# Optimization experiments

Measured on AMD Instinct MI355X. Metric: run time of the kernel, lower is better.

Reference implementation:

```python
import jax, jax.numpy as jnp
import numpy as np

B, N, D, H = 4, 4096, 1024, 16
DK = D // H


def setup_inputs() -> dict:
    key = jax.random.key(0)
    ks = jax.random.split(key, 11)
    s = 0.02  # small init scale for weights
    return {
        "query": jax.random.normal(ks[0], (B, N, D), jnp.float32),
        "key": jax.random.normal(ks[1], (B, N, D), jnp.float32),
        "value": jax.random.normal(ks[2], (B, N, D), jnp.float32),
        "Wq": jax.random.normal(ks[3], (D, D), jnp.float32) * s,
        "bq": jax.random.normal(ks[4], (D,), jnp.float32) * s,
        "Wk": jax.random.normal(ks[5], (D, D), jnp.float32) * s,
        "bk": jax.random.normal(ks[6], (D,), jnp.float32) * s,
        "Wv": jax.random.normal(ks[7], (D, D), jnp.float32) * s,
        "bv": jax.random.normal(ks[8], (D,), jnp.float32) * s,
        "Wo": jax.random.normal(ks[9], (D, D), jnp.float32) * s,
        "bo": jax.random.normal(ks[10], (D,), jnp.float32) * s,
    }


def reference(query, key, value, Wq, bq, Wk, bk, Wv, bv, Wo, bo):
    b, n, d = query.shape
    h, dk = H, d // H

    def proj(x, W, bias):
        # torch Linear: y = x @ W.T + b ; then split heads -> [b,h,n,dk]
        y = x @ W.T + bias
        return y.reshape(b, n, h, dk).transpose(0, 2, 1, 3)

    q = proj(query, Wq, bq)
    k = proj(key, Wk, bk)
    v = proj(value, Wv, bv)

    # linear attention (Efficient Attention, arXiv:1812.01243)
    q = jax.nn.softmax(q, axis=-1) * (1.0 / np.sqrt(dk).astype(np.float32))
    k = jax.nn.softmax(k, axis=-2)  # softmax over sequence dim
    ctx = jnp.einsum('bhnd,bhne->bhde', k, v)   # [b,h,dk,dk]
    out = jnp.einsum('bhnd,bhde->bhne', q, ctx)  # [b,h,n,dk]

    out = out.transpose(0, 2, 1, 3).reshape(b, n, d)
    return out @ Wo.T + bo
```

## Files before the change

### kernel.cpp

```cpp
#include <hip/hip_runtime.h>
#include <hip/hip_bf16.h>

#define B_ 4
#define N_ 4096
#define D_ 1024
#define H_ 16

typedef __attribute__((ext_vector_type(4))) float f32x4;
typedef __attribute__((ext_vector_type(8))) short s16x8;

__device__ __forceinline__ ushort f2bf(float f) {
  union { float f; unsigned u; } v; v.f = f;
  unsigned u = v.u;
  return (ushort)((u + 0x7fffu + ((u >> 16) & 1u)) >> 16);
}
__device__ __forceinline__ float bf2f(ushort h) {
  union { unsigned u; float f; } v; v.u = ((unsigned)h) << 16;
  return v.f;
}

__device__ __forceinline__ void gld16(const ushort* g, ushort* lds_base) {
  __builtin_amdgcn_global_load_lds(
      (const __attribute__((address_space(1))) unsigned int*)g,
      (__attribute__((address_space(3))) unsigned int*)lds_base, 16, 0, 0);
}

__device__ __forceinline__ s16x8 cvt8(float4 a, float4 b) {
  s16x8 o;
  o[0] = (short)f2bf(a.x); o[1] = (short)f2bf(a.y); o[2] = (short)f2bf(a.z); o[3] = (short)f2bf(a.w);
  o[4] = (short)f2bf(b.x); o[5] = (short)f2bf(b.y); o[6] = (short)f2bf(b.z); o[7] = (short)f2bf(b.w);
  return o;
}

__global__ void conv_x_kernel(const float* __restrict__ x0, const float* __restrict__ x1,
                              const float* __restrict__ x2, ushort* __restrict__ dst) {
  const int z = blockIdx.z;
  const float* src = z == 0 ? x0 : (z == 1 ? x1 : x2);
  ushort* d = dst + (long)z * 16777216;
  const long i0 = ((long)blockIdx.x * 256 + threadIdx.x) * 8;
  const long STR = (long)1024 * 256 * 8;
  float4 va[8], vb[8];
#pragma unroll
  for (int u = 0; u < 8; ++u) {
    va[u] = *(const float4*)(src + i0 + u * STR);
    vb[u] = *(const float4*)(src + i0 + u * STR + 4);
  }
#pragma unroll
  for (int u = 0; u < 8; ++u) {
    *(s16x8*)(d + i0 + u * STR) = cvt8(va[u], vb[u]);
  }
}

__global__ void conv_w_kernel(const float* __restrict__ w0, const float* __restrict__ w1,
                              const float* __restrict__ w2, const float* __restrict__ w3,
                              ushort* __restrict__ dst) {
  const int z = blockIdx.z;
  const float* src = z == 0 ? w0 : z == 1 ? w1 : z == 2 ? w2 : w3;
  ushort* d = dst + (long)z * (D_ * D_);
  const long i0 = ((long)blockIdx.x * 256 + threadIdx.x) * 8;
  const long STR = (long)128 * 256 * 8;
  float4 va[4], vb[4];
#pragma unroll
  for (int u = 0; u < 4; ++u) {
    va[u] = *(const float4*)(src + i0 + u * STR);
    vb[u] = *(const float4*)(src + i0 + u * STR + 4);
  }
#pragma unroll
  for (int u = 0; u < 4; ++u) {
    *(s16x8*)(d + i0 + u * STR) = cvt8(va[u], vb[u]);
  }
}

template <int EPI>
__global__ __launch_bounds__(256, 2) void gemm_bt_kernel(
    const ushort* __restrict__ A, const ushort* __restrict__ Bm,
    void* __restrict__ Cv, const float* __restrict__ bias, float* __restrict__ kpart,
    int M, int N, int K, long sA, long sB, long sC) {
  __shared__ ushort As[128 * 32];
  __shared__ ushort Bs[128 * 32];
  const int z = blockIdx.z;
  A += (long)z * sA; Bm += (long)z * sB;
  const int m0 = blockIdx.x * 128, n0 = blockIdx.y * 128;
  const int tid = threadIdx.x;
  const int wave = tid >> 6, lane = tid & 63;
  const int fl = lane & 15, fh = lane >> 4;
  const int wm = wave >> 1, wn = wave & 1;
  f32x4 acc[4][4] = {};
  const int c0 = tid, c1 = tid + 256;
  const int r0 = c0 >> 2, k80 = (c0 & 3) * 8;
  const int r1 = c1 >> 2, k81 = (c1 & 3) * 8;
  ushort* ldsA0 = As + wave * 512;
  ushort* ldsA1 = As + 2048 + wave * 512;
  ushort* ldsB0 = Bs + wave * 512;
  ushort* ldsB1 = Bs + 2048 + wave * 512;
  for (int kk = 0; kk < K; kk += 32) {
    __syncthreads();
    gld16(A + (long)(m0 + r0) * K + kk + k80, ldsA0);
    gld16(A + (long)(m0 + r1) * K + kk + k81, ldsA1);
    gld16(Bm + (long)(n0 + r0) * K + kk + k80, ldsB0);
    gld16(Bm + (long)(n0 + r1) * K + kk + k81, ldsB1);
    __syncthreads();
    s16x8 fa[4], fb[4];
#pragma unroll
    for (int i = 0; i < 4; ++i)
      fa[i] = *(const s16x8*)(As + (wm * 64 + i * 16 + fl) * 32 + fh * 8);
#pragma unroll
    for (int j = 0; j < 4; ++j)
      fb[j] = *(const s16x8*)(Bs + (wn * 64 + j * 16 + fl) * 32 + fh * 8);
#pragma unroll
    for (int i = 0; i < 4; ++i)
#pragma unroll
      for (int j = 0; j < 4; ++j)
        acc[i][j] = __builtin_amdgcn_mfma_f32_16x16x32_bf16(fa[i], fb[j], acc[i][j], 0, 0, 0);
  }

  if constexpr (EPI == 0) {
    ushort* C = (ushort*)Cv;
#pragma unroll
    for (int j = 0; j < 4; ++j) {
      int col = n0 + wn * 64 + j * 16 + fl;
#pragma unroll
      for (int i = 0; i < 4; ++i)
#pragma unroll
        for (int r = 0; r < 4; ++r) {
          int row = m0 + wm * 64 + i * 16 + fh * 4 + r;
          C[(long)row * N + col] = f2bf(acc[i][j][r]);
        }
    }
  } else if constexpr (EPI == 1) {
    ushort* C = (ushort*)Cv;
    float bcol[4];
#pragma unroll
    for (int j = 0; j < 4; ++j) bcol[j] = bias[n0 + wn * 64 + j * 16 + fl];
#pragma unroll
    for (int i = 0; i < 4; ++i)
#pragma unroll
      for (int r = 0; r < 4; ++r) {
        float v[4];
#pragma unroll
        for (int j = 0; j < 4; ++j) v[j] = acc[i][j][r] + bcol[j];
        float m = fmaxf(fmaxf(v[0], v[1]), fmaxf(v[2], v[3]));
#pragma unroll
        for (int o = 1; o <= 8; o <<= 1) m = fmaxf(m, __shfl_xor(m, o));
        float e[4], s = 0.f;
#pragma unroll
        for (int j = 0; j < 4; ++j) { e[j] = __expf(v[j] - m); s += e[j]; }
#pragma unroll
        for (int o = 1; o <= 8; o <<= 1) s += __shfl_xor(s, o);
        float sc = 0.125f / s;
        int row = m0 + wm * 64 + i * 16 + fh * 4 + r;
#pragma unroll
        for (int j = 0; j < 4; ++j)
          C[(long)row * N + n0 + wn * 64 + j * 16 + fl] = f2bf(e[j] * sc);
      }
  } else if constexpr (EPI == 2) {
    ushort* C = (ushort*)Cv;
    float csum[4] = {};
#pragma unroll
    for (int j = 0; j < 4; ++j) {
      int col = n0 + wn * 64 + j * 16 + fl;
#pragma unroll
      for (int i = 0; i < 4; ++i)
#pragma unroll
        for (int r = 0; r < 4; ++r) {
          int row = m0 + wm * 64 + i * 16 + fh * 4 + r;
          float e = __expf(acc[i][j][r]);
          csum[j] += e;
          C[(long)row * N + col] = f2bf(e);
        }
    }
#pragma unroll
    for (int j = 0; j < 4; ++j) {
#pragma unroll
      for (int o = 16; o <= 32; o <<= 1) csum[j] += __shfl_xor(csum[j], o);
    }
    if (fh == 0) {
      int b = m0 >> 12;
      int chunk = ((m0 & 4095) >> 7) * 2 + wm;
#pragma unroll
      for (int j = 0; j < 4; ++j)
        kpart[(long)b * 65536 + (long)chunk * 1024 + n0 + wn * 64 + j * 16 + fl] = csum[j];
    }
  } else {
    float* C = (float*)Cv + (long)z * sC;
#pragma unroll
    for (int j = 0; j < 4; ++j) {
      int col = n0 + wn * 64 + j * 16 + fl;
      float bv = bias[col];
#pragma unroll
      for (int i = 0; i < 4; ++i)
#pragma unroll
        for (int r = 0; r < 4; ++r) {
          int row = m0 + wm * 64 + i * 16 + fh * 4 + r;
          C[(long)row * N + col] = acc[i][j][r] + bv;
        }
    }
  }
}

__global__ void ksm2_kernel(const float* __restrict__ kpart, float* __restrict__ colinv) {
  int idx = blockIdx.x * 256 + threadIdx.x;
  int b = idx >> 10, d = idx & 1023;
  float s = 0.f;
  for (int c = 0; c < 64; ++c) s += kpart[(long)b * 65536 + (long)c * 1024 + d];
  colinv[idx] = 1.0f / s;
}

__global__ __launch_bounds__(256, 2) void ctx_partial_kernel(
    const ushort* __restrict__ Ksm, const ushort* __restrict__ Vp, float* __restrict__ part) {
  __shared__ ushort Ks[128 * 64];
  __shared__ ushort Vs[128 * 64];
  const int chunk = blockIdx.x;
  const int bh = blockIdx.y;
  const int b = bh >> 4, h = bh & 15;
  const int tid = threadIdx.x, wave = tid >> 6, lane = tid & 63;
  const int fl = lane & 15, fh = lane >> 4;
  f32x4 acc[4] = {};
  for (int t = 0; t < 4; ++t) {
    const long base = ((long)(b * N_ + chunk * 512 + t * 128)) * D_ + h * 64;
    __syncthreads();
#pragma unroll
    for (int i = 0; i < 4; ++i) {
      int c = i * 256 + tid;
      int r = c >> 3, k8 = (c & 7) * 8;
      ushort* lk = Ks + (long)(i * 256 + wave * 64) * 8;
      ushort* lv = Vs + (long)(i * 256 + wave * 64) * 8;
      gld16(Ksm + base + (long)r * D_ + k8, lk);
      gld16(Vp + base + (long)r * D_ + k8, lv);
    }
    __syncthreads();
#pragma unroll
    for (int s = 0; s < 4; ++s) {
      s16x8 fa;
#pragma unroll
      for (int j = 0; j < 8; ++j)
        fa[j] = (short)Ks[(s * 32 + fh * 8 + j) * 64 + wave * 16 + fl];
#pragma unroll
      for (int jt = 0; jt < 4; ++jt) {
        s16x8 fb;
#pragma unroll
        for (int j = 0; j < 8; ++j)
          fb[j] = (short)Vs[(s * 32 + fh * 8 + j) * 64 + jt * 16 + fl];
        acc[jt] = __builtin_amdgcn_mfma_f32_16x16x32_bf16(fa, fb, acc[jt], 0, 0, 0);
      }
    }
  }
  float* dst = part + ((long)chunk * 64 + bh) * 4096;
#pragma unroll
  for (int jt = 0; jt < 4; ++jt)
#pragma unroll
    for (int r = 0; r < 4; ++r)
      dst[(wave * 16 + fh * 4 + r) * 64 + jt * 16 + fl] = acc[jt][r];
}

__global__ void ctx_reduce_kernel(const float* __restrict__ part, const float* __restrict__ bv,
                                  const float* __restrict__ colinv, ushort* __restrict__ ctxb) {
  int idx = blockIdx.x * 256 + threadIdx.x;
  int e = idx & 63;
  int dk = (idx >> 6) & 63;
  int h = (idx >> 12) & 15;
  int b = idx >> 16;
  float s = 0.f;
#pragma unroll
  for (int c = 0; c < 8; ++c) s += part[(long)c * 262144 + idx];
  ctxb[idx] = f2bf(s * colinv[b * 1024 + h * 64 + dk] + bv[h * 64 + e]);
}

__global__ __launch_bounds__(256, 2) void mb_kernel(
    const ushort* __restrict__ Wob, const ushort* __restrict__ ctxb, ushort* __restrict__ Mb) {
  const int o0 = blockIdx.x * 64, h = blockIdx.y, b = blockIdx.z;
  const int tid = threadIdx.x, wave = tid >> 6, lane = tid & 63;
  const int fl = lane & 15, fh = lane >> 4;
  const ushort* ctxh = ctxb + ((long)(b * 16 + h)) * 4096;
  f32x4 acc[4] = {};
#pragma unroll
  for (int s = 0; s < 2; ++s) {
    s16x8 fa = *(const s16x8*)(Wob + (long)(o0 + wave * 16 + fl) * D_ + h * 64 + s * 32 + fh * 8);
#pragma unroll
    for (int jt = 0; jt < 4; ++jt) {
      s16x8 fb = *(const s16x8*)(ctxh + (long)(jt * 16 + fl) * 64 + s * 32 + fh * 8);
      acc[jt] = __builtin_amdgcn_mfma_f32_16x16x32_bf16(fa, fb, acc[jt], 0, 0, 0);
    }
  }
  ushort* dst = Mb + (long)b * (D_ * D_);
#pragma unroll
  for (int jt = 0; jt < 4; ++jt)
#pragma unroll
    for (int r = 0; r < 4; ++r)
      dst[(long)(o0 + wave * 16 + fh * 4 + r) * D_ + h * 64 + jt * 16 + fl] = f2bf(acc[jt][r]);
}

extern "C" void kernel_launch(void* const* d_in, const int* in_sizes, int n_in,
                              void* d_out, int out_size, void* d_ws, size_t ws_size,
                              hipStream_t stream) {
  const float* q_in = (const float*)d_in[0];
  const float* k_in = (const float*)d_in[1];
  const float* v_in = (const float*)d_in[2];
  const float* Wq = (const float*)d_in[3];
  const float* bq = (const float*)d_in[4];
  const float* Wk = (const float*)d_in[5];
  const float* Wv = (const float*)d_in[7];
  const float* bv = (const float*)d_in[8];
  const float* Wo = (const float*)d_in[9];
  const float* bo = (const float*)d_in[10];

  char* ws = (char*)d_ws;
  ushort* Xq = (ushort*)(ws + 0);
  ushort* Xk = (ushort*)(ws + 33554432);
  ushort* Xv = (ushort*)(ws + 67108864);
  ushort* Wb = (ushort*)(ws + 100663296);
  ushort* Qp = (ushort*)(ws + 109051904);
  ushort* Kp = (ushort*)(ws + 142606336);
  ushort* Vp = (ushort*)(ws + 176160768);
  float* kpart = (float*)(ws + 0);
  float* colinv = (float*)(ws + 1048576);
  float* ctxpart = (float*)(ws + 2097152);
  ushort* ctxb = (ushort*)(ws + 10485760);
  ushort* Mb = (ushort*)(ws + 11534336);

  ushort* Wbq = Wb;
  ushort* Wbk = Wb + 1048576;
  ushort* Wbv = Wb + 2097152;
  ushort* Wbo = Wb + 3145728;

  conv_w_kernel<<<dim3(128, 1, 4), 256, 0, stream>>>(Wq, Wk, Wv, Wo, Wb);
  conv_x_kernel<<<dim3(1024, 1, 3), 256, 0, stream>>>(q_in, k_in, v_in, Xq);

  gemm_bt_kernel<1><<<dim3(128, 8, 1), 256, 0, stream>>>(
      Xq, Wbq, Qp, bq, nullptr, 16384, 1024, 1024, 0, 0, 0);
  gemm_bt_kernel<2><<<dim3(128, 8, 1), 256, 0, stream>>>(
      Xk, Wbk, Kp, nullptr, kpart, 16384, 1024, 1024, 0, 0, 0);
  gemm_bt_kernel<0><<<dim3(128, 8, 1), 256, 0, stream>>>(
      Xv, Wbv, Vp, nullptr, nullptr, 16384, 1024, 1024, 0, 0, 0);

  ksm2_kernel<<<16, 256, 0, stream>>>(kpart, colinv);

  ctx_partial_kernel<<<dim3(8, 64), 256, 0, stream>>>(Kp, Vp, ctxpart);
  ctx_reduce_kernel<<<1024, 256, 0, stream>>>(ctxpart, bv, colinv, ctxb);
  mb_kernel<<<dim3(16, 16, 4), 256, 0, stream>>>(Wbo, ctxb, Mb);

  gemm_bt_kernel<3><<<dim3(32, 8, 4), 256, 0, stream>>>(
      Qp, Mb, (float*)d_out, bo, nullptr, 4096, 1024, 1024,
      (long)4096 * 1024, (long)1024 * 1024, (long)4096 * 1024);
}
```

Measured before the change: 292.7 us.

## Fuse fp32-to-bf16 activation conversion into projection GEMM A-tile loads

Removes the separate activation conversion kernel. The three projection GEMMs now read fp32 inputs directly, convert them to bf16 in registers with a packed convert instruction, and write the result to LDS. The next A tile is prefetched into registers during the current iteration. Block indices are remapped so each XCD owns a contiguous band of M tiles, which is meant to improve L2 reuse. In exchange, fp32 A reads double the A-side load bytes per GEMM, and the register-staged path replaces the async global-to-LDS loads.

```diff
diff --git a/kernel.cpp b/kernel.cpp
--- a/kernel.cpp
+++ b/kernel.cpp
@@ -14,10 +14,6 @@
   unsigned u = v.u;
   return (ushort)((u + 0x7fffu + ((u >> 16) & 1u)) >> 16);
 }
-__device__ __forceinline__ float bf2f(ushort h) {
-  union { unsigned u; float f; } v; v.u = ((unsigned)h) << 16;
-  return v.f;
-}
 
 __device__ __forceinline__ void gld16(const ushort* g, ushort* lds_base) {
   __builtin_amdgcn_global_load_lds(
@@ -25,30 +21,10 @@
       (__attribute__((address_space(3))) unsigned int*)lds_base, 16, 0, 0);
 }
 
-__device__ __forceinline__ s16x8 cvt8(float4 a, float4 b) {
-  s16x8 o;
-  o[0] = (short)f2bf(a.x); o[1] = (short)f2bf(a.y); o[2] = (short)f2bf(a.z); o[3] = (short)f2bf(a.w);
-  o[4] = (short)f2bf(b.x); o[5] = (short)f2bf(b.y); o[6] = (short)f2bf(b.z); o[7] = (short)f2bf(b.w);
-  return o;
-}
-
-__global__ void conv_x_kernel(const float* __restrict__ x0, const float* __restrict__ x1,
-                              const float* __restrict__ x2, ushort* __restrict__ dst) {
-  const int z = blockIdx.z;
-  const float* src = z == 0 ? x0 : (z == 1 ? x1 : x2);
-  ushort* d = dst + (long)z * 16777216;
-  const long i0 = ((long)blockIdx.x * 256 + threadIdx.x) * 8;
-  const long STR = (long)1024 * 256 * 8;
-  float4 va[8], vb[8];
-#pragma unroll
-  for (int u = 0; u < 8; ++u) {
-    va[u] = *(const float4*)(src + i0 + u * STR);
-    vb[u] = *(const float4*)(src + i0 + u * STR + 4);
-  }
-#pragma unroll
-  for (int u = 0; u < 8; ++u) {
-    *(s16x8*)(d + i0 + u * STR) = cvt8(va[u], vb[u]);
-  }
+__device__ __forceinline__ unsigned cvtpk(float lo, float hi) {
+  unsigned r;
+  asm("v_cvt_pk_bf16_f32 %0, %1, %2" : "=v"(r) : "v"(lo), "v"(hi));
+  return r;
 }
 
 __global__ void conv_w_kernel(const float* __restrict__ w0, const float* __restrict__ w1,
@@ -59,46 +35,75 @@
   ushort* d = dst + (long)z * (D_ * D_);
   const long i0 = ((long)blockIdx.x * 256 + threadIdx.x) * 8;
   const long STR = (long)128 * 256 * 8;
-  float4 va[4], vb[4];
 #pragma unroll
   for (int u = 0; u < 4; ++u) {
-    va[u] = *(const float4*)(src + i0 + u * STR);
-    vb[u] = *(const float4*)(src + i0 + u * STR + 4);
-  }
-#pragma unroll
-  for (int u = 0; u < 4; ++u) {
-    *(s16x8*)(d + i0 + u * STR) = cvt8(va[u], vb[u]);
-  }
-}
-
-template <int EPI>
+    f32x4 a = *(const f32x4*)(src + i0 + u * STR);
+    f32x4 b = *(const f32x4*)(src + i0 + u * STR + 4);
+    s16x8 o;
+    o[0] = (short)f2bf(a[0]); o[1] = (short)f2bf(a[1]); o[2] = (short)f2bf(a[2]); o[3] = (short)f2bf(a[3]);
+    o[4] = (short)f2bf(b[0]); o[5] = (short)f2bf(b[1]); o[6] = (short)f2bf(b[2]); o[7] = (short)f2bf(b[3]);
+    *(s16x8*)(d + i0 + u * STR) = o;
+  }
+}
+
+template <int EPI, bool AFP32>
 __global__ __launch_bounds__(256, 2) void gemm_bt_kernel(
-    const ushort* __restrict__ A, const ushort* __restrict__ Bm,
+    const void* __restrict__ Av, const ushort* __restrict__ Bm,
     void* __restrict__ Cv, const float* __restrict__ bias, float* __restrict__ kpart,
-    int M, int N, int K, long sA, long sB, long sC) {
+    int MT, int K, long sA, long sB, long sC) {
   __shared__ ushort As[128 * 32];
   __shared__ ushort Bs[128 * 32];
   const int z = blockIdx.z;
-  A += (long)z * sA; Bm += (long)z * sB;
-  const int m0 = blockIdx.x * 128, n0 = blockIdx.y * 128;
+  Bm += (long)z * sB;
+  const int lin = blockIdx.x;
+  const int xcd = lin & 7, idx = lin >> 3;
+  const int mpx = MT >> 3;
+  const int m0 = (xcd * mpx + (idx >> 3)) * 128;
+  const int n0 = (idx & 7) * 128;
+  const int N = 1024;
   const int tid = threadIdx.x;
   const int wave = tid >> 6, lane = tid & 63;
   const int fl = lane & 15, fh = lane >> 4;
   const int wm = wave >> 1, wn = wave & 1;
   f32x4 acc[4][4] = {};
-  const int c0 = tid, c1 = tid + 256;
-  const int r0 = c0 >> 2, k80 = (c0 & 3) * 8;
-  const int r1 = c1 >> 2, k81 = (c1 & 3) * 8;
+  const int rb0 = tid >> 2, kb0 = (tid & 3) * 8;
+  const int rb1 = (tid + 256) >> 2, kb1 = ((tid + 256) & 3) * 8;
+  ushort* ldsB0 = Bs + wave * 512;
+  ushort* ldsB1 = Bs + 2048 + wave * 512;
   ushort* ldsA0 = As + wave * 512;
   ushort* ldsA1 = As + 2048 + wave * 512;
-  ushort* ldsB0 = Bs + wave * 512;
-  ushort* ldsB1 = Bs + 2048 + wave * 512;
+
+  const float* Af = (const float*)Av;
+  const ushort* Ab = (const ushort*)Av + (long)z * sA;
+  const float* ap = AFP32 ? (Af + (long)(m0 + (tid >> 3)) * K + (tid & 7) * 4) : nullptr;
+  ushort* wp = As + (tid >> 3) * 32 + (tid & 7) * 4;
+  f32x4 areg[4];
+  if constexpr (AFP32) {
+#pragma unroll
+    for (int u = 0; u < 4; ++u) areg[u] = *(const f32x4*)(ap + u * 32 * 1024);
+  }
+
   for (int kk = 0; kk < K; kk += 32) {
     __syncthreads();
-    gld16(A + (long)(m0 + r0) * K + kk + k80, ldsA0);
-    gld16(A + (long)(m0 + r1) * K + kk + k81, ldsA1);
-    gld16(Bm + (long)(n0 + r0) * K + kk + k80, ldsB0);
-    gld16(Bm + (long)(n0 + r1) * K + kk + k81, ldsB1);
+    gld16(Bm + (long)(n0 + rb0) * K + kk + kb0, ldsB0);
+    gld16(Bm + (long)(n0 + rb1) * K + kk + kb1, ldsB1);
+    if constexpr (AFP32) {
+#pragma unroll
+      for (int u = 0; u < 4; ++u) {
+        uint2 w;
+        w.x = cvtpk(areg[u][0], areg[u][1]);
+        w.y = cvtpk(areg[u][2], areg[u][3]);
+        *(uint2*)(wp + u * 1024) = w;
+      }
+      if (kk + 32 < K) {
+#pragma unroll
+        for (int u = 0; u < 4; ++u)
+          areg[u] = *(const f32x4*)(ap + u * 32 * 1024 + kk + 32);
+      }
+    } else {
+      gld16(Ab + (long)(m0 + rb0) * K + kk + kb0, ldsA0);
+      gld16(Ab + (long)(m0 + rb1) * K + kk + kb1, ldsA1);
+    }
     __syncthreads();
     s16x8 fa[4], fb[4];
 #pragma unroll
@@ -305,18 +310,15 @@
   const float* bo = (const float*)d_in[10];
 
   char* ws = (char*)d_ws;
-  ushort* Xq = (ushort*)(ws + 0);
-  ushort* Xk = (ushort*)(ws + 33554432);
-  ushort* Xv = (ushort*)(ws + 67108864);
-  ushort* Wb = (ushort*)(ws + 100663296);
-  ushort* Qp = (ushort*)(ws + 109051904);
-  ushort* Kp = (ushort*)(ws + 142606336);
-  ushort* Vp = (ushort*)(ws + 176160768);
-  float* kpart = (float*)(ws + 0);
-  float* colinv = (float*)(ws + 1048576);
-  float* ctxpart = (float*)(ws + 2097152);
-  ushort* ctxb = (ushort*)(ws + 10485760);
-  ushort* Mb = (ushort*)(ws + 11534336);
+  ushort* Wb = (ushort*)(ws + 0);
+  ushort* Qp = (ushort*)(ws + 8388608);
+  ushort* Kp = (ushort*)(ws + 41943040);
+  ushort* Vp = (ushort*)(ws + 75497472);
+  float* kpart = (float*)(ws + 109051904);
+  float* colinv = (float*)(ws + 110100480);
+  float* ctxpart = (float*)(ws + 110116864);
+  ushort* ctxb = (ushort*)(ws + 118505472);
+  ushort* Mb = (ushort*)(ws + 119029760);
 
   ushort* Wbq = Wb;
   ushort* Wbk = Wb + 1048576;
@@ -324,14 +326,13 @@
   ushort* Wbo = Wb + 3145728;
 
   conv_w_kernel<<<dim3(128, 1, 4), 256, 0, stream>>>(Wq, Wk, Wv, Wo, Wb);
-  conv_x_kernel<<<dim3(1024, 1, 3), 256, 0, stream>>>(q_in, k_in, v_in, Xq);
-
-  gemm_bt_kernel<1><<<dim3(128, 8, 1), 256, 0, stream>>>(
-      Xq, Wbq, Qp, bq, nullptr, 16384, 1024, 1024, 0, 0, 0);
-  gemm_bt_kernel<2><<<dim3(128, 8, 1), 256, 0, stream>>>(
-      Xk, Wbk, Kp, nullptr, kpart, 16384, 1024, 1024, 0, 0, 0);
-  gemm_bt_kernel<0><<<dim3(128, 8, 1), 256, 0, stream>>>(
-      Xv, Wbv, Vp, nullptr, nullptr, 16384, 1024, 1024, 0, 0, 0);
+
+  gemm_bt_kernel<1, true><<<dim3(1024, 1, 1), 256, 0, stream>>>(
+      q_in, Wbq, Qp, bq, nullptr, 128, 1024, 0, 0, 0);
+  gemm_bt_kernel<2, true><<<dim3(1024, 1, 1), 256, 0, stream>>>(
+      k_in, Wbk, Kp, nullptr, kpart, 128, 1024, 0, 0, 0);
+  gemm_bt_kernel<0, true><<<dim3(1024, 1, 1), 256, 0, stream>>>(
+      v_in, Wbv, Vp, nullptr, nullptr, 128, 1024, 0, 0, 0);
 
   ksm2_kernel<<<16, 256, 0, stream>>>(kpart, colinv);
 
@@ -339,7 +340,7 @@
   ctx_reduce_kernel<<<1024, 256, 0, stream>>>(ctxpart, bv, colinv, ctxb);
   mb_kernel<<<dim3(16, 16, 4), 256, 0, stream>>>(Wbo, ctxb, Mb);
 
-  gemm_bt_kernel<3><<<dim3(32, 8, 4), 256, 0, stream>>>(
-      Qp, Mb, (float*)d_out, bo, nullptr, 4096, 1024, 1024,
+  gemm_bt_kernel<3, false><<<dim3(256, 1, 4), 256, 0, stream>>>(
+      Qp, Mb, (float*)d_out, bo, nullptr, 32, 1024,
       (long)4096 * 1024, (long)1024 * 1024, (long)4096 * 1024);
 }
```

Result: faster. 263.5 us (-10.0%).
